# Kernel optimization log

Measured on AMD Instinct MI355X. Metric: run time of the kernel, lower is better.

## Reference

```python
import jax, jax.numpy as jnp
import numpy as np

B, L, V, D = 8, 128, 32000, 64
R1, R2, UP = 2 * D, 5 * D, 10 * D  # first_reduce, second_reduce, up_scale defaults


def pos_enc(seq_len, d, n=10000.0):
    # matches getPositionEncoding: P[k,2i]=sin(k/n^(2i/d)), P[k,2i+1]=cos(k/n^(2i/d))
    k = jnp.arange(seq_len, dtype=jnp.float32)[:, None]
    i = jnp.arange(d // 2, dtype=jnp.float32)[None, :]
    ang = k / (n ** (2.0 * i / d))
    return jnp.stack([jnp.sin(ang), jnp.cos(ang)], axis=-1).reshape(seq_len, d)


def setup_inputs() -> dict:
    key = jax.random.key(0)
    ks = jax.random.split(key, 20)

    def lin(k, out_f, in_f):
        bound = 1.0 / np.sqrt(in_f)
        k1, k2 = jax.random.split(k)
        W = jax.random.uniform(k1, (out_f, in_f), jnp.float32, -bound, bound)
        b = jax.random.uniform(k2, (out_f,), jnp.float32, -bound, bound)
        return W, b

    inp = {"x": jax.random.uniform(ks[0], (B, L, V), jnp.float32)}
    inp["W_emb"], inp["b_emb"] = lin(ks[1], D, V)
    inp["W_pos1"], inp["b_pos1"] = lin(ks[2], D, 2 * D)
    inp["W_red"], inp["b_red"] = lin(ks[3], R1, L * D)
    inp["W_pos2"], inp["b_pos2"] = lin(ks[4], R1, 2 * R1)
    inp["W_red2"], inp["b_red2"] = lin(ks[5], R2, L * R1)
    inp["W_pos3"], inp["b_pos3"] = lin(ks[6], R2, 2 * R2)
    inp["W_up1"], inp["b_up1"] = lin(ks[7], UP, R2)
    inp["W_up2"], inp["b_up2"] = lin(ks[8], V, UP)
    inp["W_fin"], inp["b_fin"] = lin(ks[9], 1, L)
    return inp


def reference(x, W_emb, b_emb, W_pos1, b_pos1, W_red, b_red, W_pos2, b_pos2,
              W_red2, b_red2, W_pos3, b_pos3, W_up1, b_up1, W_up2, b_up2,
              W_fin, b_fin):
    relu = jax.nn.relu
    P1 = pos_enc(L, 2 * D)   # [L, 2D]
    P2 = pos_enc(L, 2 * R1)  # [L, 2*R1]
    P3 = pos_enc(L, 2 * R2)  # [L, 2*R2]

    h = relu(x @ W_emb.T + b_emb)                       # [B, L, D]
    h = h + relu(P1 @ W_pos1.T + b_pos1)[None]          # learned sin pos emb

    # einsum('bij,bkm->bikj'): out[b,i,k,j] = h[b,i,j] * sum_m h[b,k,m]
    s = h.sum(-1)                                       # [B, L]
    h = (h[:, :, None, :] * s[:, None, :, None]).reshape(B, L, L * D)
    h = relu(h @ W_red.T + b_red)                       # [B, L, R1]
    h = h + relu(P2 @ W_pos2.T + b_pos2)[None]

    s = h.sum(-1)                                       # [B, L]
    h = (h[:, :, None, :] * s[:, None, :, None]).reshape(B, L, L * R1)
    h = relu(h @ W_red2.T + b_red2)                     # [B, L, R2]
    h = h + relu(P3 @ W_pos3.T + b_pos3)[None]

    h = relu(h @ W_up1.T + b_up1)                       # [B, L, UP]
    h = relu(h @ W_up2.T + b_up2)                       # [B, L, V]
    # transpose(1,2) then Linear(L->1), relu, squeeze
    out = relu(jnp.einsum('blv,l->bv', h, W_fin[0]) + b_fin[0])  # [B, V]
    return out
```

## Files before the change

kernel.cpp:

```cpp
#include <hip/hip_runtime.h>
#include <hip/hip_bf16.h>
#include <math.h>

#define B_  8
#define L_  128
#define V_  32000
#define D_  64
#define R1_ 128
#define R2_ 320
#define UP_ 640
#define SPLITS_ 50

typedef short bf16x8 __attribute__((ext_vector_type(8)));
typedef float f32x4 __attribute__((ext_vector_type(4)));

#define GLDS16(gp, lp)                                                         \
    __builtin_amdgcn_global_load_lds(                                          \
        (const __attribute__((address_space(1))) void*)(gp),                   \
        (__attribute__((address_space(3))) void*)(lp), 16, 0, 0)

static __device__ inline unsigned short f2bf(float x) {
    __hip_bfloat16 h = __float2bfloat16(x);
    return *reinterpret_cast<unsigned short*>(&h);
}

static __device__ inline void split1(float v, unsigned short& h, unsigned short& l) {
    unsigned short hb = f2bf(v);
    float hf = __uint_as_float(((unsigned int)hb) << 16);
    h = hb;
    l = f2bf(v - hf);
}

__global__ __launch_bounds__(320) void prep_all(const float* __restrict__ Wemb,
                                                unsigned short* __restrict__ Whb,
                                                unsigned short* __restrict__ Wlb,
                                                const float* __restrict__ Wup2,
                                                unsigned short* __restrict__ Wup2b,
                                                const float* __restrict__ W1,
                                                const float* __restrict__ b1,
                                                float* __restrict__ o1,
                                                const float* __restrict__ W2,
                                                const float* __restrict__ b2,
                                                float* __restrict__ o2,
                                                const float* __restrict__ W3,
                                                const float* __restrict__ b3,
                                                float* __restrict__ o3) {
    __shared__ float P[640];
    int bx = blockIdx.x, t = threadIdx.x;
    if (bx < 800) {
        int u = bx * 320 + t;
        int kb = u >> 6, row = u & 63;
        const float* s = Wemb + (size_t)row * 32000 + kb * 8;
        unsigned short h8[8], l8[8];
#pragma unroll
        for (int j = 0; j < 8; ++j) split1(s[j], h8[j], l8[j]);
        *(ushort4*)&Whb[(size_t)u * 8]     = *(ushort4*)&h8[0];
        *(ushort4*)&Whb[(size_t)u * 8 + 4] = *(ushort4*)&h8[4];
        *(ushort4*)&Wlb[(size_t)u * 8]     = *(ushort4*)&l8[0];
        *(ushort4*)&Wlb[(size_t)u * 8 + 4] = *(ushort4*)&l8[4];
    } else if (bx < 1184) {
        int id = bx - 800;
        int l = id & 127;
        int stage = id >> 7;
        const float* W = (stage == 0) ? W1 : (stage == 1) ? W2 : W3;
        const float* bias = (stage == 0) ? b1 : (stage == 1) ? b2 : b3;
        float* out = (stage == 0) ? o1 : (stage == 1) ? o2 : o3;
        int outF = (stage == 0) ? 64 : (stage == 1) ? 128 : 320;
        int dEnc = 2 * outF;
        for (int m = t; m < dEnc; m += 320) {
            int i = m >> 1;
            float ang = (float)l * powf(10000.0f, -2.0f * (float)i / (float)dEnc);
            P[m] = (m & 1) ? cosf(ang) : sinf(ang);
        }
        __syncthreads();
        if (t < outF) {
            float acc = bias[t];
            const float4* w = (const float4*)(W + (size_t)t * dEnc);
            for (int m4 = 0; m4 < dEnc / 4; ++m4) {
                float4 wv = w[m4];
                float4 pv = *(const float4*)&P[m4 * 4];
                acc = fmaf(pv.x, wv.x, acc);
                acc = fmaf(pv.y, wv.y, acc);
                acc = fmaf(pv.z, wv.z, acc);
                acc = fmaf(pv.w, wv.w, acc);
            }
            out[l * outF + t] = fmaxf(acc, 0.f);
        }
    } else {
        const int n4 = (V_ * UP_) / 4;
        int stride = 3200 * 320;
        for (int i = (bx - 1184) * 320 + t; i < n4; i += stride) {
            float4 v = ((const float4*)Wup2)[i];
            ushort4 o;
            o.x = f2bf(v.x); o.y = f2bf(v.y); o.z = f2bf(v.z); o.w = f2bf(v.w);
            ((ushort4*)Wup2b)[i] = o;
        }
    }
}

__global__ __launch_bounds__(256) void embA_mfma(const float* __restrict__ x,
                                                 const unsigned short* __restrict__ Whb,
                                                 const unsigned short* __restrict__ Wlb,
                                                 float* __restrict__ partA) {
    __shared__ short lds[16384];
    int t = threadIdx.x;
    int lane = t & 63, w = t >> 6;
    int ln = lane & 15, lg = lane >> 4;
    int rb = blockIdx.x, ks = blockIdx.y;
    int row0 = rb * 64;
    const float* xrow = x + (size_t)(row0 + w * 16 + ln) * 32000;

    f32x4 acc[4];
#pragma unroll
    for (int nt = 0; nt < 4; ++nt) acc[nt] = (f32x4){0.f, 0.f, 0.f, 0.f};

    float4 xc[4], xn[4];
    {
        int kb0 = (ks * 640) >> 3;
#pragma unroll
        for (int s = 0; s < 4; ++s) {
            int ubase = s * 256 + w * 64;
            const unsigned short* arr = (s < 2) ? Whb : Wlb;
            int uu = (s < 2) ? ubase : (ubase - 512);
            const char* gp = (const char*)arr + ((size_t)kb0 * 64 + uu + lane) * 16;
            char* lp = (char*)lds + ((s < 2) ? 0 : 8192) + uu * 16;
            GLDS16(gp, lp);
        }
        const float* bp = xrow + ks * 640 + lg * 8;
        xc[0] = ((const float4*)bp)[0];
        xc[1] = ((const float4*)bp)[1];
        xc[2] = ((const float4*)(bp + 32))[0];
        xc[3] = ((const float4*)(bp + 32))[1];
    }

#pragma unroll 2
    for (int ch = 0; ch < 10; ++ch) {
        __syncthreads();
        if (ch < 9) {
            int kb0 = (ks * 640 + (ch + 1) * 64) >> 3;
            int p = (ch + 1) & 1;
#pragma unroll
            for (int s = 0; s < 4; ++s) {
                int ubase = s * 256 + w * 64;
                const unsigned short* arr = (s < 2) ? Whb : Wlb;
                int uu = (s < 2) ? ubase : (ubase - 512);
                const char* gp = (const char*)arr + ((size_t)kb0 * 64 + uu + lane) * 16;
                char* lp = (char*)lds + p * 16384 + ((s < 2) ? 0 : 8192) + uu * 16;
                GLDS16(gp, lp);
            }
            const float* bp = xrow + ks * 640 + (ch + 1) * 64 + lg * 8;
            xn[0] = ((const float4*)bp)[0];
            xn[1] = ((const float4*)bp)[1];
            xn[2] = ((const float4*)(bp + 32))[0];
            xn[3] = ((const float4*)(bp + 32))[1];
        }
        bf16x8 ah[2], al[2];
#pragma unroll
        for (int kstep = 0; kstep < 2; ++kstep) {
            float f[8] = {xc[2 * kstep].x, xc[2 * kstep].y, xc[2 * kstep].z, xc[2 * kstep].w,
                          xc[2 * kstep + 1].x, xc[2 * kstep + 1].y, xc[2 * kstep + 1].z,
                          xc[2 * kstep + 1].w};
            unsigned short h8[8], l8[8];
#pragma unroll
            for (int j = 0; j < 8; ++j) split1(f[j], h8[j], l8[j]);
            ah[kstep] = *(bf16x8*)h8;
            al[kstep] = *(bf16x8*)l8;
        }
        const char* buf = (const char*)lds + (ch & 1) * 16384;
#pragma unroll
        for (int kstep = 0; kstep < 2; ++kstep) {
            int g = kstep * 4 + lg;
#pragma unroll
            for (int nt = 0; nt < 4; ++nt) {
                int nrow = nt * 16 + ln;
                bf16x8 bh = *(const bf16x8*)(buf + (g * 64 + nrow) * 16);
                bf16x8 bl = *(const bf16x8*)(buf + 8192 + (g * 64 + nrow) * 16);
                acc[nt] = __builtin_amdgcn_mfma_f32_16x16x32_bf16(ah[kstep], bh, acc[nt], 0, 0, 0);
                acc[nt] = __builtin_amdgcn_mfma_f32_16x16x32_bf16(ah[kstep], bl, acc[nt], 0, 0, 0);
                acc[nt] = __builtin_amdgcn_mfma_f32_16x16x32_bf16(al[kstep], bh, acc[nt], 0, 0, 0);
            }
        }
#pragma unroll
        for (int i = 0; i < 4; ++i) xc[i] = xn[i];
    }
#pragma unroll
    for (int nt = 0; nt < 4; ++nt)
#pragma unroll
        for (int r = 0; r < 4; ++r)
            partA[((size_t)ks * 1024 + row0 + w * 16 + lg * 4 + r) * 64 + nt * 16 + ln] =
                acc[nt][r];
}

__global__ __launch_bounds__(64) void reduceA_kernel(const float* __restrict__ partA,
                                                     const float* __restrict__ bemb,
                                                     const float* __restrict__ pe1,
                                                     float* __restrict__ h1,
                                                     float* __restrict__ s1) {
    int row = blockIdx.x;
    int d = threadIdx.x;
    int l = row & 127;
    float v = bemb[d];
#pragma unroll 10
    for (int s = 0; s < SPLITS_; ++s) v += partA[((size_t)s * 1024 + row) * 64 + d];
    v = fmaxf(v, 0.f) + pe1[l * 64 + d];
    h1[row * 64 + d] = v;
    float sum = v;
    for (int off = 32; off > 0; off >>= 1) sum += __shfl_down(sum, off);
    if (d == 0) s1[row] = sum;
}

__global__ __launch_bounds__(64) void wr1_kernel(const float* __restrict__ Wred,
                                                 const float* __restrict__ s1,
                                                 float* __restrict__ Wr1) {
    __shared__ float ss[8 * 128];
    int r = blockIdx.x;
    int j = threadIdx.x;
    for (int idx = j; idx < 1024; idx += 64) ss[idx] = s1[idx];
    __syncthreads();
    float acc[8];
#pragma unroll
    for (int b = 0; b < 8; ++b) acc[b] = 0.f;
    const float* w = Wred + (size_t)r * 8192 + j;
#pragma unroll 8
    for (int k = 0; k < 128; ++k) {
        float wv = w[k * 64];
#pragma unroll
        for (int b = 0; b < 8; ++b) acc[b] = fmaf(ss[b * 128 + k], wv, acc[b]);
    }
#pragma unroll
    for (int b = 0; b < 8; ++b) Wr1[((size_t)b * 128 + r) * 64 + j] = acc[b];
}

__global__ __launch_bounds__(128) void h2_kernel(const float* __restrict__ h1,
                                                 const float* __restrict__ Wr1,
                                                 const float* __restrict__ bred,
                                                 const float* __restrict__ pe2,
                                                 float* __restrict__ h2,
                                                 float* __restrict__ s2) {
    __shared__ float hrow[64];
    __shared__ float red[2];
    int row = blockIdx.x;
    int b = row >> 7, i = row & 127;
    int r = threadIdx.x;
    if (r < 64) hrow[r] = h1[row * 64 + r];
    __syncthreads();
    float acc = bred[r];
    const float4* w = (const float4*)(Wr1 + ((size_t)b * 128 + r) * 64);
#pragma unroll
    for (int j4 = 0; j4 < 16; ++j4) {
        float4 wv = w[j4];
        float4 hv = *(const float4*)&hrow[j4 * 4];
        acc = fmaf(hv.x, wv.x, acc);
        acc = fmaf(hv.y, wv.y, acc);
        acc = fmaf(hv.z, wv.z, acc);
        acc = fmaf(hv.w, wv.w, acc);
    }
    float val = fmaxf(acc, 0.f) + pe2[i * 128 + r];
    h2[row * 128 + r] = val;
    float sum = val;
    for (int off = 32; off > 0; off >>= 1) sum += __shfl_down(sum, off);
    if ((r & 63) == 0) red[r >> 6] = sum;
    __syncthreads();
    if (r == 0) s2[row] = red[0] + red[1];
}

__global__ __launch_bounds__(128) void wr2_kernel(const float* __restrict__ Wred2,
                                                  const float* __restrict__ s2,
                                                  float* __restrict__ Wr2) {
    __shared__ float ss[8 * 128];
    int r = blockIdx.x;
    int j = threadIdx.x;
    for (int idx = j; idx < 1024; idx += 128) ss[idx] = s2[idx];
    __syncthreads();
    float acc[8];
#pragma unroll
    for (int b = 0; b < 8; ++b) acc[b] = 0.f;
    const float* w = Wred2 + (size_t)r * 16384 + j;
#pragma unroll 8
    for (int k = 0; k < 128; ++k) {
        float wv = w[k * 128];
#pragma unroll
        for (int b = 0; b < 8; ++b) acc[b] = fmaf(ss[b * 128 + k], wv, acc[b]);
    }
#pragma unroll
    for (int b = 0; b < 8; ++b) Wr2[((size_t)b * 320 + r) * 128 + j] = acc[b];
}

__global__ __launch_bounds__(320) void h3_kernel(const float* __restrict__ h2,
                                                 const float* __restrict__ Wr2,
                                                 const float* __restrict__ bred2,
                                                 const float* __restrict__ pe3,
                                                 float* __restrict__ h3) {
    __shared__ float hrow[128];
    int row = blockIdx.x;
    int b = row >> 7, i = row & 127;
    int r = threadIdx.x;
    if (r < 128) hrow[r] = h2[row * 128 + r];
    __syncthreads();
    float acc = bred2[r];
    const float4* w = (const float4*)(Wr2 + ((size_t)b * 320 + r) * 128);
#pragma unroll
    for (int j4 = 0; j4 < 32; ++j4) {
        float4 wv = w[j4];
        float4 hv = *(const float4*)&hrow[j4 * 4];
        acc = fmaf(hv.x, wv.x, acc);
        acc = fmaf(hv.y, wv.y, acc);
        acc = fmaf(hv.z, wv.z, acc);
        acc = fmaf(hv.w, wv.w, acc);
    }
    h3[(size_t)row * 320 + r] = fmaxf(acc, 0.f) + pe3[i * 320 + r];
}

__global__ __launch_bounds__(320) void h4_kernel(const float* __restrict__ h3,
                                                 const float* __restrict__ Wup1,
                                                 const float* __restrict__ bup1,
                                                 unsigned short* __restrict__ h4b) {
    __shared__ float hsT[320 * 4];
    int t = threadIdx.x;
    int row0 = blockIdx.x * 4;
    int u = blockIdx.y * 320 + t;
    for (int idx = t; idx < 1280; idx += 320) {
        int q = idx / 320, j = idx - q * 320;
        hsT[j * 4 + q] = h3[(size_t)(row0 + q) * 320 + j];
    }
    __syncthreads();
    float acc[4] = {0.f, 0.f, 0.f, 0.f};
    const float4* w = (const float4*)(Wup1 + (size_t)u * 320);
#pragma unroll 2
    for (int j4 = 0; j4 < 80; ++j4) {
        float4 wv = w[j4];
#pragma unroll
        for (int e = 0; e < 4; ++e) {
            float wc = (e == 0) ? wv.x : (e == 1) ? wv.y : (e == 2) ? wv.z : wv.w;
            float4 hv = *(const float4*)&hsT[(j4 * 4 + e) * 4];
            acc[0] = fmaf(hv.x, wc, acc[0]);
            acc[1] = fmaf(hv.y, wc, acc[1]);
            acc[2] = fmaf(hv.z, wc, acc[2]);
            acc[3] = fmaf(hv.w, wc, acc[3]);
        }
    }
    float bias = bup1[u];
#pragma unroll
    for (int q = 0; q < 4; ++q)
        h4b[(size_t)(row0 + q) * 640 + u] = f2bf(fmaxf(acc[q] + bias, 0.f));
}

__global__ __launch_bounds__(512) void final_mfma_kernel(
    const unsigned short* __restrict__ h4b,
    const unsigned short* __restrict__ Wup2b,
    const float* __restrict__ bup2,
    const float* __restrict__ Wfin,
    const float* __restrict__ bfin,
    float* __restrict__ out) {
    __shared__ short tile[2][12288];
    __shared__ float redbuf[2][2][128];

    int t = threadIdx.x;
    int lane = t & 63;
    int w = t >> 6;
    int wv = w >> 2;
    int wq = w & 3;
    int bl_ = wq >> 1, lh = wq & 1;
    int ln = lane & 15, lg = lane >> 4;
    int b0 = blockIdx.y * 2;
    int v0 = blockIdx.x * 128;

    f32x4 acc[4][4];
#pragma unroll
    for (int mt = 0; mt < 4; ++mt)
#pragma unroll
        for (int nt = 0; nt < 4; ++nt) acc[mt][nt] = (f32x4){0.f, 0.f, 0.f, 0.f};

    auto stage = [&](int ch, int p) {
#pragma unroll
        for (int s = 0; s < 3; ++s) {
            int F = (w * 3 + s) * 1024 + lane * 16;
            int region = F >> 13;
            int rr = (F >> 6) & 127;
            int g = ((F >> 4) & 3) ^ (rr & 3);
            size_t rowG = (region == 0) ? (size_t)(v0 + rr)
                                        : (size_t)((b0 + region - 1) * 128 + rr);
            const unsigned short* base = (region == 0) ? Wup2b : h4b;
            const char* gp =
                (const char*)base + (rowG * 640 + (size_t)(ch * 32 + g * 8)) * 2;
            char* lp = (char*)&tile[p][0] + (w * 3 + s) * 1024;
            GLDS16(gp, lp);
        }
    };

    stage(0, 0);

#pragma unroll 2
    for (int ch = 0; ch < 20; ++ch) {
        __syncthreads();
        if (ch < 19) stage(ch + 1, (ch + 1) & 1);
        const char* buf = (const char*)&tile[ch & 1][0];
        bf16x8 aF[4], bF[4];
#pragma unroll
        for (int mt = 0; mt < 4; ++mt) {
            int rA = wv * 64 + mt * 16 + ln;
            aF[mt] = *(const bf16x8*)(buf + rA * 64 + ((lg ^ (rA & 3)) * 16));
        }
#pragma unroll
        for (int nt = 0; nt < 4; ++nt) {
            int rB = lh * 64 + nt * 16 + ln;
            bF[nt] = *(const bf16x8*)(buf + 8192 * (1 + bl_) + rB * 64 +
                                      ((lg ^ (rB & 3)) * 16));
        }
#pragma unroll
        for (int mt = 0; mt < 4; ++mt)
#pragma unroll
            for (int nt = 0; nt < 4; ++nt)
                acc[mt][nt] = __builtin_amdgcn_mfma_f32_16x16x32_bf16(
                    aF[mt], bF[nt], acc[mt][nt], 0, 0, 0);
    }

    float bfin0 = bfin[0];
#pragma unroll
    for (int mt = 0; mt < 4; ++mt) {
        float bu[4];
#pragma unroll
        for (int r = 0; r < 4; ++r)
            bu[r] = bup2[v0 + wv * 64 + mt * 16 + lg * 4 + r];
        float part[4] = {0.f, 0.f, 0.f, 0.f};
#pragma unroll
        for (int nt = 0; nt < 4; ++nt) {
            float wf = Wfin[lh * 64 + nt * 16 + ln];
#pragma unroll
            for (int r = 0; r < 4; ++r)
                part[r] += wf * fmaxf(acc[mt][nt][r] + bu[r], 0.f);
        }
#pragma unroll
        for (int off = 8; off >= 1; off >>= 1)
#pragma unroll
            for (int r = 0; r < 4; ++r) part[r] += __shfl_xor(part[r], off, 64);
        if (ln == 0) {
#pragma unroll
            for (int r = 0; r < 4; ++r)
                redbuf[bl_][lh][wv * 64 + mt * 16 + lg * 4 + r] = part[r];
        }
    }
    __syncthreads();
    if (t < 256) {
        int bb = t >> 7, v = t & 127;
        float vsum = redbuf[bb][0][v] + redbuf[bb][1][v] + bfin0;
        out[(size_t)(b0 + bb) * 32000 + v0 + v] = fmaxf(vsum, 0.f);
    }
}

extern "C" void kernel_launch(void* const* d_in, const int* in_sizes, int n_in,
                              void* d_out, int out_size, void* d_ws, size_t ws_size,
                              hipStream_t stream) {
    const float* x      = (const float*)d_in[0];
    const float* W_emb  = (const float*)d_in[1];
    const float* b_emb  = (const float*)d_in[2];
    const float* W_pos1 = (const float*)d_in[3];
    const float* b_pos1 = (const float*)d_in[4];
    const float* W_red  = (const float*)d_in[5];
    const float* b_red  = (const float*)d_in[6];
    const float* W_pos2 = (const float*)d_in[7];
    const float* b_pos2 = (const float*)d_in[8];
    const float* W_red2 = (const float*)d_in[9];
    const float* b_red2 = (const float*)d_in[10];
    const float* W_pos3 = (const float*)d_in[11];
    const float* b_pos3 = (const float*)d_in[12];
    const float* W_up1  = (const float*)d_in[13];
    const float* b_up1  = (const float*)d_in[14];
    const float* W_up2  = (const float*)d_in[15];
    const float* b_up2  = (const float*)d_in[16];
    const float* W_fin  = (const float*)d_in[17];
    const float* b_fin  = (const float*)d_in[18];
    float* out = (float*)d_out;

    float* ws  = (float*)d_ws;
    float* pe1 = ws;
    float* pe2 = pe1 + 8192;
    float* pe3 = pe2 + 16384;
    float* h1  = pe3 + 40960;
    float* s1  = h1 + 65536;
    float* Wr1 = s1 + 1024;
    float* h2  = Wr1 + 65536;
    float* s2  = h2 + 131072;
    float* Wr2 = s2 + 1024;
    float* h3  = Wr2 + 327680;
    unsigned short* h4b   = (unsigned short*)(h3 + 327680);
    unsigned short* Wup2b = (unsigned short*)((float*)h4b + 327680);
    float* after = (float*)Wup2b + 10240000;
    unsigned short* Whb = (unsigned short*)after;
    unsigned short* Wlb = Whb + 2048000;
    float* partA = (float*)(Wlb + 2048000);

    prep_all<<<dim3(4384), 320, 0, stream>>>(W_emb, Whb, Wlb, W_up2, Wup2b,
                                             W_pos1, b_pos1, pe1, W_pos2, b_pos2,
                                             pe2, W_pos3, b_pos3, pe3);
    embA_mfma<<<dim3(16, SPLITS_), 256, 0, stream>>>(x, Whb, Wlb, partA);
    reduceA_kernel<<<dim3(1024), 64, 0, stream>>>(partA, b_emb, pe1, h1, s1);
    wr1_kernel<<<dim3(128), 64, 0, stream>>>(W_red, s1, Wr1);
    h2_kernel<<<dim3(1024), 128, 0, stream>>>(h1, Wr1, b_red, pe2, h2, s2);
    wr2_kernel<<<dim3(320), 128, 0, stream>>>(W_red2, s2, Wr2);
    h3_kernel<<<dim3(1024), 320, 0, stream>>>(h2, Wr2, b_red2, pe3, h3);
    h4_kernel<<<dim3(256, 2), 320, 0, stream>>>(h3, W_up1, b_up1, h4b);
    final_mfma_kernel<<<dim3(250, 4), 512, 0, stream>>>(h4b, Wup2b, b_up2, W_fin,
                                                        b_fin, out);
}
```

Baseline: 463.8 us.

## Fuse h3/h4 kernels, split-K the wr reductions, vectorize reduceA, reorder final grid

Merges the h3 and h4 kernels into one that computes four h3 rows into shared memory and immediately applies W_up1, so the h3 intermediate never goes through global memory. Splits the k-loops in wr1/wr2 across more threads with a shared-memory partial reduction to raise parallelism. Vectorizes reduceA to float4 so each block handles four rows. Swaps the final kernel's grid axes so blocks sharing a W_up2 tile run adjacently, which should improve L2 reuse. The fused kernel has only 256 blocks and serial loops over 320/640 outputs per thread, which could leave the GPU underused.

```diff
diff --git a/kernel.cpp b/kernel.cpp
--- a/kernel.cpp
+++ b/kernel.cpp
@@ -196,39 +196,57 @@
                                                      const float* __restrict__ pe1,
                                                      float* __restrict__ h1,
                                                      float* __restrict__ s1) {
-    int row = blockIdx.x;
-    int d = threadIdx.x;
-    int l = row & 127;
-    float v = bemb[d];
+    int lane = threadIdx.x;
+    int row = blockIdx.x * 4 + (lane >> 4);
+    int d0 = (lane & 15) * 4;
+    float4 v = *(const float4*)&bemb[d0];
 #pragma unroll 10
-    for (int s = 0; s < SPLITS_; ++s) v += partA[((size_t)s * 1024 + row) * 64 + d];
-    v = fmaxf(v, 0.f) + pe1[l * 64 + d];
-    h1[row * 64 + d] = v;
-    float sum = v;
-    for (int off = 32; off > 0; off >>= 1) sum += __shfl_down(sum, off);
-    if (d == 0) s1[row] = sum;
-}
-
-__global__ __launch_bounds__(64) void wr1_kernel(const float* __restrict__ Wred,
-                                                 const float* __restrict__ s1,
-                                                 float* __restrict__ Wr1) {
-    __shared__ float ss[8 * 128];
-    int r = blockIdx.x;
-    int j = threadIdx.x;
-    for (int idx = j; idx < 1024; idx += 64) ss[idx] = s1[idx];
-    __syncthreads();
+    for (int s = 0; s < SPLITS_; ++s) {
+        float4 p = *(const float4*)&partA[((size_t)s * 1024 + row) * 64 + d0];
+        v.x += p.x; v.y += p.y; v.z += p.z; v.w += p.w;
+    }
+    float4 pe = *(const float4*)&pe1[(row & 127) * 64 + d0];
+    v.x = fmaxf(v.x, 0.f) + pe.x;
+    v.y = fmaxf(v.y, 0.f) + pe.y;
+    v.z = fmaxf(v.z, 0.f) + pe.z;
+    v.w = fmaxf(v.w, 0.f) + pe.w;
+    *(float4*)&h1[row * 64 + d0] = v;
+    float sum = v.x + v.y + v.z + v.w;
+#pragma unroll
+    for (int off = 8; off >= 1; off >>= 1) sum += __shfl_down(sum, off);
+    if ((lane & 15) == 0) s1[row] = sum;
+}
+
+__global__ __launch_bounds__(256) void wr1_kernel(const float* __restrict__ Wred,
+                                                  const float* __restrict__ s1,
+                                                  float* __restrict__ Wr1) {
+    __shared__ float ss[1024];
+    __shared__ float pl[2048];
+    int t = threadIdx.x, bb = blockIdx.x;
+    for (int i = t; i < 1024; i += 256) ss[i] = s1[i];
+    __syncthreads();
+    int r = bb >> 1, jh = bb & 1;
+    int jj = t & 31, ks = t >> 5;
+    int j = jh * 32 + jj;
     float acc[8];
 #pragma unroll
     for (int b = 0; b < 8; ++b) acc[b] = 0.f;
     const float* w = Wred + (size_t)r * 8192 + j;
-#pragma unroll 8
-    for (int k = 0; k < 128; ++k) {
+#pragma unroll
+    for (int kk = 0; kk < 16; ++kk) {
+        int k = ks * 16 + kk;
         float wv = w[k * 64];
 #pragma unroll
         for (int b = 0; b < 8; ++b) acc[b] = fmaf(ss[b * 128 + k], wv, acc[b]);
     }
 #pragma unroll
-    for (int b = 0; b < 8; ++b) Wr1[((size_t)b * 128 + r) * 64 + j] = acc[b];
+    for (int b = 0; b < 8; ++b) pl[t * 8 + b] = acc[b];
+    __syncthreads();
+    int jj2 = t >> 3, b2 = t & 7;
+    float sum = 0.f;
+#pragma unroll
+    for (int k2 = 0; k2 < 8; ++k2) sum += pl[(k2 * 32 + jj2) * 8 + b2];
+    Wr1[((size_t)b2 * 128 + r) * 64 + jh * 32 + jj2] = sum;
 }
 
 __global__ __launch_bounds__(128) void h2_kernel(const float* __restrict__ h1,
@@ -264,85 +282,100 @@
     if (r == 0) s2[row] = red[0] + red[1];
 }
 
-__global__ __launch_bounds__(128) void wr2_kernel(const float* __restrict__ Wred2,
+__global__ __launch_bounds__(256) void wr2_kernel(const float* __restrict__ Wred2,
                                                   const float* __restrict__ s2,
                                                   float* __restrict__ Wr2) {
-    __shared__ float ss[8 * 128];
-    int r = blockIdx.x;
-    int j = threadIdx.x;
-    for (int idx = j; idx < 1024; idx += 128) ss[idx] = s2[idx];
-    __syncthreads();
+    __shared__ float ss[1024];
+    __shared__ float pl[2048];
+    int t = threadIdx.x, r = blockIdx.x;
+    for (int i = t; i < 1024; i += 256) ss[i] = s2[i];
+    __syncthreads();
+    int j = t & 127, ks = t >> 7;
     float acc[8];
 #pragma unroll
     for (int b = 0; b < 8; ++b) acc[b] = 0.f;
     const float* w = Wred2 + (size_t)r * 16384 + j;
-#pragma unroll 8
-    for (int k = 0; k < 128; ++k) {
+#pragma unroll 16
+    for (int kk = 0; kk < 64; ++kk) {
+        int k = ks * 64 + kk;
         float wv = w[k * 128];
 #pragma unroll
         for (int b = 0; b < 8; ++b) acc[b] = fmaf(ss[b * 128 + k], wv, acc[b]);
     }
 #pragma unroll
-    for (int b = 0; b < 8; ++b) Wr2[((size_t)b * 320 + r) * 128 + j] = acc[b];
-}
-
-__global__ __launch_bounds__(320) void h3_kernel(const float* __restrict__ h2,
-                                                 const float* __restrict__ Wr2,
-                                                 const float* __restrict__ bred2,
-                                                 const float* __restrict__ pe3,
-                                                 float* __restrict__ h3) {
-    __shared__ float hrow[128];
-    int row = blockIdx.x;
-    int b = row >> 7, i = row & 127;
-    int r = threadIdx.x;
-    if (r < 128) hrow[r] = h2[row * 128 + r];
-    __syncthreads();
-    float acc = bred2[r];
-    const float4* w = (const float4*)(Wr2 + ((size_t)b * 320 + r) * 128);
-#pragma unroll
-    for (int j4 = 0; j4 < 32; ++j4) {
-        float4 wv = w[j4];
-        float4 hv = *(const float4*)&hrow[j4 * 4];
-        acc = fmaf(hv.x, wv.x, acc);
-        acc = fmaf(hv.y, wv.y, acc);
-        acc = fmaf(hv.z, wv.z, acc);
-        acc = fmaf(hv.w, wv.w, acc);
-    }
-    h3[(size_t)row * 320 + r] = fmaxf(acc, 0.f) + pe3[i * 320 + r];
-}
-
-__global__ __launch_bounds__(320) void h4_kernel(const float* __restrict__ h3,
-                                                 const float* __restrict__ Wup1,
-                                                 const float* __restrict__ bup1,
-                                                 unsigned short* __restrict__ h4b) {
-    __shared__ float hsT[320 * 4];
+    for (int b = 0; b < 8; ++b) pl[t * 8 + b] = acc[b];
+    __syncthreads();
+#pragma unroll
+    for (int ii = 0; ii < 4; ++ii) {
+        int idx = t * 4 + ii;
+        int j2 = idx >> 3, b2 = idx & 7;
+        float sum = pl[j2 * 8 + b2] + pl[(128 + j2) * 8 + b2];
+        Wr2[((size_t)b2 * 320 + r) * 128 + j2] = sum;
+    }
+}
+
+__global__ __launch_bounds__(256) void h3h4_kernel(const float* __restrict__ h2,
+                                                   const float* __restrict__ Wr2,
+                                                   const float* __restrict__ bred2,
+                                                   const float* __restrict__ pe3,
+                                                   const float* __restrict__ Wup1,
+                                                   const float* __restrict__ bup1,
+                                                   unsigned short* __restrict__ h4b) {
+    __shared__ float h2r[512];
+    __shared__ float hsT[1280];
     int t = threadIdx.x;
     int row0 = blockIdx.x * 4;
-    int u = blockIdx.y * 320 + t;
-    for (int idx = t; idx < 1280; idx += 320) {
-        int q = idx / 320, j = idx - q * 320;
-        hsT[j * 4 + q] = h3[(size_t)(row0 + q) * 320 + j];
-    }
-    __syncthreads();
-    float acc[4] = {0.f, 0.f, 0.f, 0.f};
-    const float4* w = (const float4*)(Wup1 + (size_t)u * 320);
+    int b = row0 >> 7;
+    h2r[t] = h2[(size_t)row0 * 128 + t];
+    h2r[t + 256] = h2[(size_t)row0 * 128 + t + 256];
+    __syncthreads();
+    int i_ = row0 & 127;
+    for (int r = t; r < 320; r += 256) {
+        const float4* w = (const float4*)(Wr2 + ((size_t)b * 320 + r) * 128);
+        float a0 = bred2[r], a1 = a0, a2 = a0, a3 = a0;
+#pragma unroll
+        for (int j4 = 0; j4 < 32; ++j4) {
+            float4 wv = w[j4];
+            float4 q0 = *(const float4*)&h2r[0 * 128 + j4 * 4];
+            float4 q1 = *(const float4*)&h2r[1 * 128 + j4 * 4];
+            float4 q2 = *(const float4*)&h2r[2 * 128 + j4 * 4];
+            float4 q3 = *(const float4*)&h2r[3 * 128 + j4 * 4];
+            a0 = fmaf(q0.x, wv.x, a0); a0 = fmaf(q0.y, wv.y, a0);
+            a0 = fmaf(q0.z, wv.z, a0); a0 = fmaf(q0.w, wv.w, a0);
+            a1 = fmaf(q1.x, wv.x, a1); a1 = fmaf(q1.y, wv.y, a1);
+            a1 = fmaf(q1.z, wv.z, a1); a1 = fmaf(q1.w, wv.w, a1);
+            a2 = fmaf(q2.x, wv.x, a2); a2 = fmaf(q2.y, wv.y, a2);
+            a2 = fmaf(q2.z, wv.z, a2); a2 = fmaf(q2.w, wv.w, a2);
+            a3 = fmaf(q3.x, wv.x, a3); a3 = fmaf(q3.y, wv.y, a3);
+            a3 = fmaf(q3.z, wv.z, a3); a3 = fmaf(q3.w, wv.w, a3);
+        }
+        hsT[r * 4 + 0] = fmaxf(a0, 0.f) + pe3[(i_ + 0) * 320 + r];
+        hsT[r * 4 + 1] = fmaxf(a1, 0.f) + pe3[(i_ + 1) * 320 + r];
+        hsT[r * 4 + 2] = fmaxf(a2, 0.f) + pe3[(i_ + 2) * 320 + r];
+        hsT[r * 4 + 3] = fmaxf(a3, 0.f) + pe3[(i_ + 3) * 320 + r];
+    }
+    __syncthreads();
+    for (int u = t; u < 640; u += 256) {
+        float acc[4] = {0.f, 0.f, 0.f, 0.f};
+        const float4* w = (const float4*)(Wup1 + (size_t)u * 320);
 #pragma unroll 2
-    for (int j4 = 0; j4 < 80; ++j4) {
-        float4 wv = w[j4];
-#pragma unroll
-        for (int e = 0; e < 4; ++e) {
-            float wc = (e == 0) ? wv.x : (e == 1) ? wv.y : (e == 2) ? wv.z : wv.w;
-            float4 hv = *(const float4*)&hsT[(j4 * 4 + e) * 4];
-            acc[0] = fmaf(hv.x, wc, acc[0]);
-            acc[1] = fmaf(hv.y, wc, acc[1]);
-            acc[2] = fmaf(hv.z, wc, acc[2]);
-            acc[3] = fmaf(hv.w, wc, acc[3]);
-        }
-    }
-    float bias = bup1[u];
-#pragma unroll
-    for (int q = 0; q < 4; ++q)
-        h4b[(size_t)(row0 + q) * 640 + u] = f2bf(fmaxf(acc[q] + bias, 0.f));
+        for (int j4 = 0; j4 < 80; ++j4) {
+            float4 wv = w[j4];
+#pragma unroll
+            for (int e = 0; e < 4; ++e) {
+                float wc = (e == 0) ? wv.x : (e == 1) ? wv.y : (e == 2) ? wv.z : wv.w;
+                float4 hv = *(const float4*)&hsT[(j4 * 4 + e) * 4];
+                acc[0] = fmaf(hv.x, wc, acc[0]);
+                acc[1] = fmaf(hv.y, wc, acc[1]);
+                acc[2] = fmaf(hv.z, wc, acc[2]);
+                acc[3] = fmaf(hv.w, wc, acc[3]);
+            }
+        }
+        float bias = bup1[u];
+#pragma unroll
+        for (int q = 0; q < 4; ++q)
+            h4b[(size_t)(row0 + q) * 640 + u] = f2bf(fmaxf(acc[q] + bias, 0.f));
+    }
 }
 
 __global__ __launch_bounds__(512) void final_mfma_kernel(
@@ -362,8 +395,8 @@
     int wq = w & 3;
     int bl_ = wq >> 1, lh = wq & 1;
     int ln = lane & 15, lg = lane >> 4;
-    int b0 = blockIdx.y * 2;
-    int v0 = blockIdx.x * 128;
+    int b0 = blockIdx.x * 2;
+    int v0 = blockIdx.y * 128;
 
     f32x4 acc[4][4];
 #pragma unroll
@@ -494,12 +527,12 @@
                                              W_pos1, b_pos1, pe1, W_pos2, b_pos2,
                                              pe2, W_pos3, b_pos3, pe3);
     embA_mfma<<<dim3(16, SPLITS_), 256, 0, stream>>>(x, Whb, Wlb, partA);
-    reduceA_kernel<<<dim3(1024), 64, 0, stream>>>(partA, b_emb, pe1, h1, s1);
-    wr1_kernel<<<dim3(128), 64, 0, stream>>>(W_red, s1, Wr1);
+    reduceA_kernel<<<dim3(256), 64, 0, stream>>>(partA, b_emb, pe1, h1, s1);
+    wr1_kernel<<<dim3(256), 256, 0, stream>>>(W_red, s1, Wr1);
     h2_kernel<<<dim3(1024), 128, 0, stream>>>(h1, Wr1, b_red, pe2, h2, s2);
-    wr2_kernel<<<dim3(320), 128, 0, stream>>>(W_red2, s2, Wr2);
-    h3_kernel<<<dim3(1024), 320, 0, stream>>>(h2, Wr2, b_red2, pe3, h3);
-    h4_kernel<<<dim3(256, 2), 320, 0, stream>>>(h3, W_up1, b_up1, h4b);
-    final_mfma_kernel<<<dim3(250, 4), 512, 0, stream>>>(h4b, Wup2b, b_up2, W_fin,
+    wr2_kernel<<<dim3(320), 256, 0, stream>>>(W_red2, s2, Wr2);
+    h3h4_kernel<<<dim3(256), 256, 0, stream>>>(h2, Wr2, b_red2, pe3, W_up1,
+                                               b_up1, h4b);
+    final_mfma_kernel<<<dim3(4, 250), 512, 0, stream>>>(h4b, Wup2b, b_up2, W_fin,
                                                         b_fin, out);
 }
```

After: 449.4 us. 1.03x faster.
